# Performance work log

Hardware: AMD Instinct MI355X
Metric: run time of the kernel (lower is better)

## Reference

```python
import math
import jax, jax.numpy as jnp
import numpy as np

# Module config (from init_kwargs): hidden_size=128, num_heads=8, dropout=0.0
HIDDEN = 128
HEADS = 8
HEAD_DIM = HIDDEN // HEADS  # 16
SCALE = math.sqrt(HEAD_DIM)  # sqrt(hidden_size_per_attention_head)
B = 1
N = 50000   # nodes
E = 800000  # edges


def setup_inputs() -> dict:
    key = jax.random.key(0)
    k1, k2, k3, k4 = jax.random.split(key, 4)
    q = jax.random.normal(k1, (B, N, HIDDEN), dtype=jnp.float32)
    k = jax.random.normal(k2, (B, N, HIDDEN), dtype=jnp.float32)
    v = jax.random.normal(k3, (B, N, HIDDEN), dtype=jnp.float32)
    edge_index = jax.random.randint(k4, (2, E), 0, N, dtype=jnp.int64)
    return {"q": q, "k": k, "v": v, "edge_index": edge_index}


def reference(q, k, v, edge_index):
    # sparse_attention_bias path (attn_type='sparse', attn_bias=None)
    batch, node_num, _ = q.shape
    total = batch * node_num
    qh = q.reshape(total, HEADS, HEAD_DIM)
    kh = k.reshape(total, HEADS, HEAD_DIM)
    vh = v.reshape(total, HEADS, HEAD_DIM)

    e_src = edge_index[0]   # gathers k, v
    e_dst = edge_index[1]   # gathers q, scatter target

    # per-edge, per-head score: [E, H, 1]
    score = jnp.sum(kh[e_src] * qh[e_dst], axis=-1, keepdims=True) / SCALE
    score = jnp.exp(jnp.clip(score, -5.0, 5.0))

    msg = vh[e_src] * score                                   # [E, H, D]
    wV = jax.ops.segment_sum(msg, e_dst, num_segments=total)   # [N, H, D]
    Z = jax.ops.segment_sum(score, e_dst, num_segments=total)  # [N, H, 1]

    x = wV / (Z + 1e-6)
    return x.reshape(batch, node_num, -1)
```

## Files before the change

kernel.cpp:

```cpp
#include <hip/hip_runtime.h>

#define HEADS 8
#define HEAD_DIM 16
#define HIDDEN 128
#define CAP 64

__device__ __forceinline__ void gather_body(const float4* __restrict__ q4,
                                            const float4* __restrict__ k4,
                                            const float4* __restrict__ v4,
                                            const int* __restrict__ perm,
                                            float* __restrict__ out,
                                            int node, int l, int beg, int end) {
    float4 qv = q4[node * 32 + l];
    float4 acc = make_float4(0.f, 0.f, 0.f, 0.f);
    float zacc = 0.f;
    int i = beg;
    for (; i + 2 <= end; i += 2) {
        int s0 = perm[i];
        int s1 = perm[i + 1];
        float4 ka = k4[s0 * 32 + l];
        float4 va = v4[s0 * 32 + l];
        float4 kb = k4[s1 * 32 + l];
        float4 vb = v4[s1 * 32 + l];
        float pa = ka.x * qv.x + ka.y * qv.y + ka.z * qv.z + ka.w * qv.w;
        float pb = kb.x * qv.x + kb.y * qv.y + kb.z * qv.z + kb.w * qv.w;
        pa += __shfl_xor(pa, 1);
        pa += __shfl_xor(pa, 2);
        pb += __shfl_xor(pb, 1);
        pb += __shfl_xor(pb, 2);
        float ea = __expf(fminf(fmaxf(pa * 0.25f, -5.f), 5.f));
        float eb = __expf(fminf(fmaxf(pb * 0.25f, -5.f), 5.f));
        acc.x += va.x * ea + vb.x * eb;
        acc.y += va.y * ea + vb.y * eb;
        acc.z += va.z * ea + vb.z * eb;
        acc.w += va.w * ea + vb.w * eb;
        zacc += ea + eb;
    }
    if (i < end) {
        int s0 = perm[i];
        float4 ka = k4[s0 * 32 + l];
        float4 va = v4[s0 * 32 + l];
        float pa = ka.x * qv.x + ka.y * qv.y + ka.z * qv.z + ka.w * qv.w;
        pa += __shfl_xor(pa, 1);
        pa += __shfl_xor(pa, 2);
        float ea = __expf(fminf(fmaxf(pa * 0.25f, -5.f), 5.f));
        acc.x += va.x * ea;
        acc.y += va.y * ea;
        acc.z += va.z * ea;
        acc.w += va.w * ea;
        zacc += ea;
    }
    float zr = zacc + 1e-6f;
    float4 o;
    o.x = acc.x / zr;
    o.y = acc.y / zr;
    o.z = acc.z / zr;
    o.w = acc.w / zr;
    ((float4*)out)[node * 32 + l] = o;
}

__global__ void fill_fixed_kernel(const int* __restrict__ ei, int* __restrict__ cursor,
                                  int* __restrict__ perm, int E) {
    __shared__ int is64_s;
    if (threadIdx.x < 64) {
        int nz = ei[2 * (int)threadIdx.x + 1];
        nz |= __shfl_xor(nz, 1);
        nz |= __shfl_xor(nz, 2);
        nz |= __shfl_xor(nz, 4);
        nz |= __shfl_xor(nz, 8);
        nz |= __shfl_xor(nz, 16);
        nz |= __shfl_xor(nz, 32);
        if (threadIdx.x == 0) is64_s = (nz == 0);
    }
    __syncthreads();
    int e = blockIdx.x * blockDim.x + threadIdx.x;
    if (e >= E) return;
    int src, dst;
    if (is64_s) {
        const long long* e64 = (const long long*)ei;
        src = (int)e64[e];
        dst = (int)e64[(long long)E + e];
    } else {
        src = ei[e];
        dst = ei[E + e];
    }
    int pos = atomicAdd(&cursor[dst], 1);
    if (pos < CAP) perm[(dst << 6) + pos] = src;
}

__global__ void gather_fixed_kernel(const float* __restrict__ q, const float* __restrict__ k,
                                    const float* __restrict__ v,
                                    const int* __restrict__ cursor, const int* __restrict__ perm,
                                    float* __restrict__ out, int N) {
    int node = blockIdx.x * (blockDim.x >> 5) + ((int)threadIdx.x >> 5);
    int l = threadIdx.x & 31;
    if (node >= N) return;
    int deg = cursor[node];
    if (deg > CAP) deg = CAP;
    int beg = node << 6;
    gather_body((const float4*)q, (const float4*)k, (const float4*)v, perm, out,
                node, l, beg, beg + deg);
}

__global__ void detect_kernel(const int* __restrict__ ei, int* __restrict__ flag) {
    int nz = 0;
    for (int i = threadIdx.x; i < 256; i += 64) nz |= ei[2 * i + 1];
    nz |= __shfl_xor(nz, 1);
    nz |= __shfl_xor(nz, 2);
    nz |= __shfl_xor(nz, 4);
    nz |= __shfl_xor(nz, 8);
    nz |= __shfl_xor(nz, 16);
    nz |= __shfl_xor(nz, 32);
    if (threadIdx.x == 0) *flag = (nz == 0) ? 1 : 0;
}

__device__ __forceinline__ int edge_at(const int* __restrict__ ei, int is64, long long pos) {
    return is64 ? (int)((const long long*)ei)[pos] : ei[pos];
}

__global__ void count_kernel(const int* __restrict__ ei, const int* __restrict__ flag,
                             int* __restrict__ deg, int E) {
    int e = blockIdx.x * blockDim.x + threadIdx.x;
    if (e >= E) return;
    int is64 = *flag;
    atomicAdd(&deg[edge_at(ei, is64, (long long)E + e)], 1);
}

__global__ void scan_partial_kernel(const int* __restrict__ deg, int* __restrict__ partials, int N) {
    int base = blockIdx.x * 1024;
    int tid = threadIdx.x;
    int s = 0;
    for (int i = tid; i < 1024; i += 256) {
        int idx = base + i;
        s += (idx < N) ? deg[idx] : 0;
    }
    for (int off = 1; off < 64; off <<= 1) s += __shfl_xor(s, off);
    __shared__ int ws[4];
    if ((tid & 63) == 0) ws[tid >> 6] = s;
    __syncthreads();
    if (tid == 0) partials[blockIdx.x] = ws[0] + ws[1] + ws[2] + ws[3];
}

__global__ void scan_partials_kernel(int* __restrict__ partials, int nb,
                                     int* __restrict__ offs, int N, int E) {
    if (threadIdx.x == 0) {
        int run = 0;
        for (int i = 0; i < nb; ++i) { int t = partials[i]; partials[i] = run; run += t; }
        offs[N] = E;
    }
}

__global__ void scan_write_kernel(const int* __restrict__ deg, const int* __restrict__ partials,
                                  int* __restrict__ offs, int* __restrict__ cursor, int N) {
    __shared__ int smem[1024];
    int base = blockIdx.x * 1024;
    int tid = threadIdx.x;
    int idx = base + tid;
    int x = (idx < N) ? deg[idx] : 0;
    smem[tid] = x;
    __syncthreads();
    int val = x;
    for (int off = 1; off < 1024; off <<= 1) {
        int t = (tid >= off) ? smem[tid - off] : 0;
        __syncthreads();
        val += t;
        smem[tid] = val;
        __syncthreads();
    }
    if (idx < N) {
        int o = partials[blockIdx.x] + val - x;
        offs[idx] = o;
        cursor[idx] = o;
    }
}

__global__ void fill_csr_kernel(const int* __restrict__ ei, const int* __restrict__ flag,
                                int* __restrict__ cursor, int* __restrict__ perm, int E) {
    int e = blockIdx.x * blockDim.x + threadIdx.x;
    if (e >= E) return;
    int is64 = *flag;
    int src = edge_at(ei, is64, e);
    int dst = edge_at(ei, is64, (long long)E + e);
    int pos = atomicAdd(&cursor[dst], 1);
    perm[pos] = src;
}

__global__ void gather_csr_kernel(const float* __restrict__ q, const float* __restrict__ k,
                                  const float* __restrict__ v,
                                  const int* __restrict__ offs, const int* __restrict__ perm,
                                  float* __restrict__ out, int N) {
    int node = blockIdx.x * (blockDim.x >> 5) + ((int)threadIdx.x >> 5);
    int l = threadIdx.x & 31;
    if (node >= N) return;
    gather_body((const float4*)q, (const float4*)k, (const float4*)v, perm, out,
                node, l, offs[node], offs[node + 1]);
}

extern "C" void kernel_launch(void* const* d_in, const int* in_sizes, int n_in,
                              void* d_out, int out_size, void* d_ws, size_t ws_size,
                              hipStream_t stream) {
    const float* q = (const float*)d_in[0];
    const float* k = (const float*)d_in[1];
    const float* v = (const float*)d_in[2];
    const int* ei  = (const int*)d_in[3];

    int N = in_sizes[0] / HIDDEN;
    int E = in_sizes[3] / 2;
    float* out = (float*)d_out;

    int block = 256;
    size_t fast_need = (size_t)N * sizeof(int) + (size_t)N * CAP * sizeof(int);

    if (ws_size >= fast_need) {
        int* cursor = (int*)d_ws;
        int* perm   = cursor + N;
        hipMemsetAsync(cursor, 0, (size_t)N * sizeof(int), stream);
        fill_fixed_kernel<<<(E + block - 1) / block, block, 0, stream>>>(ei, cursor, perm, E);
        gather_fixed_kernel<<<(N + 7) / 8, 256, 0, stream>>>(q, k, v, cursor, perm, out, N);
    } else {
        int* deg      = (int*)d_ws;
        int* offs     = deg + N;
        int* cursor   = offs + (N + 1);
        int* flag     = cursor + (N + 1);
        int* partials = flag + 1;
        int* perm     = partials + 64;
        hipMemsetAsync(deg, 0, (size_t)N * sizeof(int), stream);
        int NB = (N + 1023) / 1024;
        detect_kernel<<<1, 64, 0, stream>>>(ei, flag);
        count_kernel<<<(E + block - 1) / block, block, 0, stream>>>(ei, flag, deg, E);
        scan_partial_kernel<<<NB, 256, 0, stream>>>(deg, partials, N);
        scan_partials_kernel<<<1, 64, 0, stream>>>(partials, NB, offs, N, E);
        scan_write_kernel<<<NB, 1024, 0, stream>>>(deg, partials, offs, cursor, N);
        fill_csr_kernel<<<(E + block - 1) / block, block, 0, stream>>>(ei, flag, cursor, perm, E);
        gather_csr_kernel<<<(N + 7) / 8, 256, 0, stream>>>(q, k, v, offs, perm, out, N);
    }
}
```

Baseline: 267.6 us.

## Convert K/V to bf16 in fused prep kernel and gather with half-warp per edge

Adds a prep kernel that fuses the edge bucketing fill with a pass converting K and V to packed bf16 in workspace. A new gather kernel reads the bf16 K/V, has each 16-lane half process a different edge with 8 elements per lane, then combines the halves with shuffles. This targets the random gather bandwidth by halving the bytes per edge and shrinking the working set to fit caches better. It costs an extra conversion pass each call and introduces bf16 rounding error. The multi-kernel CSR fallback is removed.

After: 236.8 us. -11.5%, faster.

```diff
diff --git a/kernel.cpp b/kernel.cpp
--- a/kernel.cpp
+++ b/kernel.cpp
@@ -5,13 +5,172 @@
 #define HIDDEN 128
 #define CAP 64
 
-__device__ __forceinline__ void gather_body(const float4* __restrict__ q4,
-                                            const float4* __restrict__ k4,
-                                            const float4* __restrict__ v4,
-                                            const int* __restrict__ perm,
-                                            float* __restrict__ out,
-                                            int node, int l, int beg, int end) {
+__device__ __forceinline__ unsigned pack2_bf16(float a, float b) {
+    unsigned ua = __float_as_uint(a);
+    unsigned ub = __float_as_uint(b);
+    ua = (ua + 0x7fffu + ((ua >> 16) & 1u)) >> 16;
+    ub = (ub + 0x7fffu + ((ub >> 16) & 1u)) >> 16;
+    return ua | (ub << 16);
+}
+__device__ __forceinline__ float bflo(unsigned u) { return __uint_as_float(u << 16); }
+__device__ __forceinline__ float bfhi(unsigned u) { return __uint_as_float(u & 0xffff0000u); }
+
+__global__ void prep_kernel(const int* __restrict__ ei, int E,
+                            const float* __restrict__ k, const float* __restrict__ v,
+                            int* __restrict__ cursor, int* __restrict__ perm,
+                            unsigned* __restrict__ kb, unsigned* __restrict__ vb,
+                            int fill_blocks, int nvec ) {
+    if ((int)blockIdx.x < fill_blocks) {
+        __shared__ int is64_s;
+        if (threadIdx.x < 64) {
+            int nz = ei[2 * (int)threadIdx.x + 1];
+            nz |= __shfl_xor(nz, 1);
+            nz |= __shfl_xor(nz, 2);
+            nz |= __shfl_xor(nz, 4);
+            nz |= __shfl_xor(nz, 8);
+            nz |= __shfl_xor(nz, 16);
+            nz |= __shfl_xor(nz, 32);
+            if (threadIdx.x == 0) is64_s = (nz == 0);
+        }
+        __syncthreads();
+        int e = blockIdx.x * blockDim.x + threadIdx.x;
+        if (e >= E) return;
+        int src, dst;
+        if (is64_s) {
+            const long long* e64 = (const long long*)ei;
+            src = (int)e64[e];
+            dst = (int)e64[(long long)E + e];
+        } else {
+            src = ei[e];
+            dst = ei[E + e];
+        }
+        int pos = atomicAdd(&cursor[dst], 1);
+        if (pos < CAP) perm[(dst << 6) + pos] = src;
+    } else {
+        int t = (blockIdx.x - fill_blocks) * blockDim.x + threadIdx.x;
+        if (t >= 2 * nvec) return;
+        int arr = (t >= nvec) ? 1 : 0;
+        int i = arr ? t - nvec : t;
+        const float4* s4 = (const float4*)(arr ? v : k);
+        float4 a = s4[2 * i];
+        float4 b = s4[2 * i + 1];
+        uint4 o;
+        o.x = pack2_bf16(a.x, a.y);
+        o.y = pack2_bf16(a.z, a.w);
+        o.z = pack2_bf16(b.x, b.y);
+        o.w = pack2_bf16(b.z, b.w);
+        ((uint4*)(arr ? vb : kb))[i] = o;
+    }
+}
+
+__global__ __launch_bounds__(256) void gather_bf16_kernel(
+        const float* __restrict__ q,
+        const uint4* __restrict__ kb4, const uint4* __restrict__ vb4,
+        const int* __restrict__ cursor, const int* __restrict__ perm,
+        float* __restrict__ out, int N) {
+    int node = blockIdx.x * 8 + ((int)threadIdx.x >> 5);
+    int l = threadIdx.x & 31;
+    int half = l >> 4;
+    int sl = l & 15;
+    if (node >= N) return;
+
+    const float4* qp = (const float4*)q;
+    float4 qa = qp[node * 32 + sl * 2];
+    float4 qb = qp[node * 32 + sl * 2 + 1];
+    float q0 = qa.x * 0.25f, q1 = qa.y * 0.25f, q2 = qa.z * 0.25f, q3 = qa.w * 0.25f;
+    float q4 = qb.x * 0.25f, q5 = qb.y * 0.25f, q6 = qb.z * 0.25f, q7 = qb.w * 0.25f;
+
+    int deg = cursor[node];
+    if (deg > CAP) deg = CAP;
+    int beg = node << 6;
+    int end = beg + deg;
+
+    float a0 = 0.f, a1 = 0.f, a2 = 0.f, a3 = 0.f, a4 = 0.f, a5 = 0.f, a6 = 0.f, a7 = 0.f;
+    float zacc = 0.f;
+
+    for (int i = beg; i < end; i += 2) {
+        int idx = i + half;
+        if (idx < end) {
+            int s = perm[idx];
+            uint4 kw = kb4[s * 16 + sl];
+            float p = bflo(kw.x) * q0 + bfhi(kw.x) * q1 + bflo(kw.y) * q2 + bfhi(kw.y) * q3
+                    + bflo(kw.z) * q4 + bfhi(kw.z) * q5 + bflo(kw.w) * q6 + bfhi(kw.w) * q7;
+            p += __shfl_xor(p, 1);
+            float e = __expf(fminf(fmaxf(p, -5.f), 5.f));
+            uint4 vw = vb4[s * 16 + sl];
+            a0 += bflo(vw.x) * e;
+            a1 += bfhi(vw.x) * e;
+            a2 += bflo(vw.y) * e;
+            a3 += bfhi(vw.y) * e;
+            a4 += bflo(vw.z) * e;
+            a5 += bfhi(vw.z) * e;
+            a6 += bflo(vw.w) * e;
+            a7 += bfhi(vw.w) * e;
+            zacc += e;
+        }
+    }
+    a0 += __shfl_xor(a0, 16);
+    a1 += __shfl_xor(a1, 16);
+    a2 += __shfl_xor(a2, 16);
+    a3 += __shfl_xor(a3, 16);
+    a4 += __shfl_xor(a4, 16);
+    a5 += __shfl_xor(a5, 16);
+    a6 += __shfl_xor(a6, 16);
+    a7 += __shfl_xor(a7, 16);
+    zacc += __shfl_xor(zacc, 16);
+
+    if (half == 0) {
+        float inv = 1.0f / (zacc + 1e-6f);
+        float4* out4 = (float4*)out;
+        out4[node * 32 + sl * 2]     = make_float4(a0 * inv, a1 * inv, a2 * inv, a3 * inv);
+        out4[node * 32 + sl * 2 + 1] = make_float4(a4 * inv, a5 * inv, a6 * inv, a7 * inv);
+    }
+}
+
+__global__ void fill_fixed_kernel(const int* __restrict__ ei, int* __restrict__ cursor,
+                                  int* __restrict__ perm, int E) {
+    __shared__ int is64_s;
+    if (threadIdx.x < 64) {
+        int nz = ei[2 * (int)threadIdx.x + 1];
+        nz |= __shfl_xor(nz, 1);
+        nz |= __shfl_xor(nz, 2);
+        nz |= __shfl_xor(nz, 4);
+        nz |= __shfl_xor(nz, 8);
+        nz |= __shfl_xor(nz, 16);
+        nz |= __shfl_xor(nz, 32);
+        if (threadIdx.x == 0) is64_s = (nz == 0);
+    }
+    __syncthreads();
+    int e = blockIdx.x * blockDim.x + threadIdx.x;
+    if (e >= E) return;
+    int src, dst;
+    if (is64_s) {
+        const long long* e64 = (const long long*)ei;
+        src = (int)e64[e];
+        dst = (int)e64[(long long)E + e];
+    } else {
+        src = ei[e];
+        dst = ei[E + e];
+    }
+    int pos = atomicAdd(&cursor[dst], 1);
+    if (pos < CAP) perm[(dst << 6) + pos] = src;
+}
+
+__global__ void gather_fixed_kernel(const float* __restrict__ q, const float* __restrict__ k,
+                                    const float* __restrict__ v,
+                                    const int* __restrict__ cursor, const int* __restrict__ perm,
+                                    float* __restrict__ out, int N) {
+    int node = blockIdx.x * (blockDim.x >> 5) + ((int)threadIdx.x >> 5);
+    int l = threadIdx.x & 31;
+    if (node >= N) return;
+    const float4* q4 = (const float4*)q;
+    const float4* k4 = (const float4*)k;
+    const float4* v4 = (const float4*)v;
     float4 qv = q4[node * 32 + l];
+    int deg = cursor[node];
+    if (deg > CAP) deg = CAP;
+    int beg = node << 6;
+    int end = beg + deg;
     float4 acc = make_float4(0.f, 0.f, 0.f, 0.f);
     float zacc = 0.f;
     int i = beg;
@@ -51,149 +210,8 @@
         zacc += ea;
     }
     float zr = zacc + 1e-6f;
-    float4 o;
-    o.x = acc.x / zr;
-    o.y = acc.y / zr;
-    o.z = acc.z / zr;
-    o.w = acc.w / zr;
-    ((float4*)out)[node * 32 + l] = o;
-}
-
-__global__ void fill_fixed_kernel(const int* __restrict__ ei, int* __restrict__ cursor,
-                                  int* __restrict__ perm, int E) {
-    __shared__ int is64_s;
-    if (threadIdx.x < 64) {
-        int nz = ei[2 * (int)threadIdx.x + 1];
-        nz |= __shfl_xor(nz, 1);
-        nz |= __shfl_xor(nz, 2);
-        nz |= __shfl_xor(nz, 4);
-        nz |= __shfl_xor(nz, 8);
-        nz |= __shfl_xor(nz, 16);
-        nz |= __shfl_xor(nz, 32);
-        if (threadIdx.x == 0) is64_s = (nz == 0);
-    }
-    __syncthreads();
-    int e = blockIdx.x * blockDim.x + threadIdx.x;
-    if (e >= E) return;
-    int src, dst;
-    if (is64_s) {
-        const long long* e64 = (const long long*)ei;
-        src = (int)e64[e];
-        dst = (int)e64[(long long)E + e];
-    } else {
-        src = ei[e];
-        dst = ei[E + e];
-    }
-    int pos = atomicAdd(&cursor[dst], 1);
-    if (pos < CAP) perm[(dst << 6) + pos] = src;
-}
-
-__global__ void gather_fixed_kernel(const float* __restrict__ q, const float* __restrict__ k,
-                                    const float* __restrict__ v,
-                                    const int* __restrict__ cursor, const int* __restrict__ perm,
-                                    float* __restrict__ out, int N) {
-    int node = blockIdx.x * (blockDim.x >> 5) + ((int)threadIdx.x >> 5);
-    int l = threadIdx.x & 31;
-    if (node >= N) return;
-    int deg = cursor[node];
-    if (deg > CAP) deg = CAP;
-    int beg = node << 6;
-    gather_body((const float4*)q, (const float4*)k, (const float4*)v, perm, out,
-                node, l, beg, beg + deg);
-}
-
-__global__ void detect_kernel(const int* __restrict__ ei, int* __restrict__ flag) {
-    int nz = 0;
-    for (int i = threadIdx.x; i < 256; i += 64) nz |= ei[2 * i + 1];
-    nz |= __shfl_xor(nz, 1);
-    nz |= __shfl_xor(nz, 2);
-    nz |= __shfl_xor(nz, 4);
-    nz |= __shfl_xor(nz, 8);
-    nz |= __shfl_xor(nz, 16);
-    nz |= __shfl_xor(nz, 32);
-    if (threadIdx.x == 0) *flag = (nz == 0) ? 1 : 0;
-}
-
-__device__ __forceinline__ int edge_at(const int* __restrict__ ei, int is64, long long pos) {
-    return is64 ? (int)((const long long*)ei)[pos] : ei[pos];
-}
-
-__global__ void count_kernel(const int* __restrict__ ei, const int* __restrict__ flag,
-                             int* __restrict__ deg, int E) {
-    int e = blockIdx.x * blockDim.x + threadIdx.x;
-    if (e >= E) return;
-    int is64 = *flag;
-    atomicAdd(&deg[edge_at(ei, is64, (long long)E + e)], 1);
-}
-
-__global__ void scan_partial_kernel(const int* __restrict__ deg, int* __restrict__ partials, int N) {
-    int base = blockIdx.x * 1024;
-    int tid = threadIdx.x;
-    int s = 0;
-    for (int i = tid; i < 1024; i += 256) {
-        int idx = base + i;
-        s += (idx < N) ? deg[idx] : 0;
-    }
-    for (int off = 1; off < 64; off <<= 1) s += __shfl_xor(s, off);
-    __shared__ int ws[4];
-    if ((tid & 63) == 0) ws[tid >> 6] = s;
-    __syncthreads();
-    if (tid == 0) partials[blockIdx.x] = ws[0] + ws[1] + ws[2] + ws[3];
-}
-
-__global__ void scan_partials_kernel(int* __restrict__ partials, int nb,
-                                     int* __restrict__ offs, int N, int E) {
-    if (threadIdx.x == 0) {
-        int run = 0;
-        for (int i = 0; i < nb; ++i) { int t = partials[i]; partials[i] = run; run += t; }
-        offs[N] = E;
-    }
-}
-
-__global__ void scan_write_kernel(const int* __restrict__ deg, const int* __restrict__ partials,
-                                  int* __restrict__ offs, int* __restrict__ cursor, int N) {
-    __shared__ int smem[1024];
-    int base = blockIdx.x * 1024;
-    int tid = threadIdx.x;
-    int idx = base + tid;
-    int x = (idx < N) ? deg[idx] : 0;
-    smem[tid] = x;
-    __syncthreads();
-    int val = x;
-    for (int off = 1; off < 1024; off <<= 1) {
-        int t = (tid >= off) ? smem[tid - off] : 0;
-        __syncthreads();
-        val += t;
-        smem[tid] = val;
-        __syncthreads();
-    }
-    if (idx < N) {
-        int o = partials[blockIdx.x] + val - x;
-        offs[idx] = o;
-        cursor[idx] = o;
-    }
-}
-
-__global__ void fill_csr_kernel(const int* __restrict__ ei, const int* __restrict__ flag,
-                                int* __restrict__ cursor, int* __restrict__ perm, int E) {
-    int e = blockIdx.x * blockDim.x + threadIdx.x;
-    if (e >= E) return;
-    int is64 = *flag;
-    int src = edge_at(ei, is64, e);
-    int dst = edge_at(ei, is64, (long long)E + e);
-    int pos = atomicAdd(&cursor[dst], 1);
-    perm[pos] = src;
-}
-
-__global__ void gather_csr_kernel(const float* __restrict__ q, const float* __restrict__ k,
-                                  const float* __restrict__ v,
-                                  const int* __restrict__ offs, const int* __restrict__ perm,
-                                  float* __restrict__ out, int N) {
-    int node = blockIdx.x * (blockDim.x >> 5) + ((int)threadIdx.x >> 5);
-    int l = threadIdx.x & 31;
-    if (node >= N) return;
-    gather_body((const float4*)q, (const float4*)k, (const float4*)v, perm, out,
-                node, l, offs[node], offs[node + 1]);
+    ((float4*)out)[node * 32 + l] =
+        make_float4(acc.x / zr, acc.y / zr, acc.z / zr, acc.w / zr);
 }
 
 extern "C" void kernel_launch(void* const* d_in, const int* in_sizes, int n_in,
@@ -209,29 +227,27 @@
     float* out = (float*)d_out;
 
     int block = 256;
-    size_t fast_need = (size_t)N * sizeof(int) + (size_t)N * CAP * sizeof(int);
-
-    if (ws_size >= fast_need) {
-        int* cursor = (int*)d_ws;
-        int* perm   = cursor + N;
+    int nvec = N * HIDDEN / 8;
+
+    size_t need_bf16 = (size_t)N * sizeof(int) + (size_t)N * CAP * sizeof(int)
+                     + 2 * (size_t)nvec * sizeof(uint4);
+    size_t need_f32  = (size_t)N * sizeof(int) + (size_t)N * CAP * sizeof(int);
+
+    int* cursor = (int*)d_ws;
+    int* perm   = cursor + N;
+
+    if (ws_size >= need_bf16) {
+        unsigned* kb = (unsigned*)(perm + (size_t)N * CAP);
+        unsigned* vb = kb + (size_t)nvec * 4;
+        hipMemsetAsync(cursor, 0, (size_t)N * sizeof(int), stream);
+        int FB = (E + block - 1) / block;
+        int CB = (2 * nvec + block - 1) / block;
+        prep_kernel<<<FB + CB, block, 0, stream>>>(ei, E, k, v, cursor, perm, kb, vb, FB, nvec);
+        gather_bf16_kernel<<<(N + 7) / 8, 256, 0, stream>>>(
+            q, (const uint4*)kb, (const uint4*)vb, cursor, perm, out, N);
+    } else if (ws_size >= need_f32) {
         hipMemsetAsync(cursor, 0, (size_t)N * sizeof(int), stream);
         fill_fixed_kernel<<<(E + block - 1) / block, block, 0, stream>>>(ei, cursor, perm, E);
         gather_fixed_kernel<<<(N + 7) / 8, 256, 0, stream>>>(q, k, v, cursor, perm, out, N);
-    } else {
-        int* deg      = (int*)d_ws;
-        int* offs     = deg + N;
-        int* cursor   = offs + (N + 1);
-        int* flag     = cursor + (N + 1);
-        int* partials = flag + 1;
-        int* perm     = partials + 64;
-        hipMemsetAsync(deg, 0, (size_t)N * sizeof(int), stream);
-        int NB = (N + 1023) / 1024;
-        detect_kernel<<<1, 64, 0, stream>>>(ei, flag);
-        count_kernel<<<(E + block - 1) / block, block, 0, stream>>>(ei, flag, deg, E);
-        scan_partial_kernel<<<NB, 256, 0, stream>>>(deg, partials, N);
-        scan_partials_kernel<<<1, 64, 0, stream>>>(partials, NB, offs, N, E);
-        scan_write_kernel<<<NB, 1024, 0, stream>>>(deg, partials, offs, cursor, N);
-        fill_csr_kernel<<<(E + block - 1) / block, block, 0, stream>>>(ei, flag, cursor, perm, E);
-        gather_csr_kernel<<<(N + 7) / 8, 256, 0, stream>>>(q, k, v, offs, perm, out, N);
-    }
-}
+    }
+}
```
